# Optimization experiments

Hardware: AMD Instinct MI355X
Metric: run time of the kernel (lower is better)

## Reference

```python
import jax, jax.numpy as jnp
import numpy as np

N_NODES = 50000


def setup_inputs() -> dict:
    key = jax.random.key(0)
    k1, k2, k3, k4, k5 = jax.random.split(key, 5)
    h = jax.random.normal(k1, (50000, 256), dtype=jnp.float32)
    norm = jax.random.uniform(k2, (50000, 1), dtype=jnp.float32)
    weight = jax.random.normal(k3, (256, 96), dtype=jnp.float32) * (1.0 / np.sqrt(96.0))
    src = jax.random.randint(k4, (800000,), 0, N_NODES, dtype=jnp.int64)
    dst = jax.random.randint(k5, (800000,), 0, N_NODES, dtype=jnp.int64)
    return {"h": h, "norm": norm, "weight": weight, "src": src, "dst": dst}


def reference(h, norm, weight, src, dst):
    # dense projection: [N, in] @ [in, out] -> [N, out]
    hw = jnp.matmul(h, weight)
    # pre-aggregation degree norm
    hw = hw * norm
    # copy_src + sum: gather messages from src, scatter-add into dst
    msgs = hw[src]  # [E, out]
    agg = jax.ops.segment_sum(msgs, dst, num_segments=N_NODES)
    # post-aggregation degree norm + activation
    out = jax.nn.relu(agg * norm)
    return out
```

## Files before the change

kernel.cpp:

```cpp
#include <hip/hip_runtime.h>

#define M_NODES 50000
#define KDIM    256
#define NDIM    96
#define NEDGE   800000
#define BM      64
#define TPB     2
#define GEMM_BLKS 391
#define NPB     64
#define NBUCK   782
#define CAPB    1536
#define EPB     2048
#define NBLK_SC 391
#define TOT_BLKS 782

typedef short bf16x8 __attribute__((ext_vector_type(8)));
typedef float f32x4  __attribute__((ext_vector_type(4)));

__device__ inline unsigned short f2bf(float x) {
    unsigned u = __float_as_uint(x);
    u = (u + 0x7fffu + ((u >> 16) & 1u)) >> 16;
    return (unsigned short)u;
}
__device__ inline unsigned pack2bf(float x, float y) {
    return (unsigned)f2bf(x) | ((unsigned)f2bf(y) << 16);
}

__global__ __launch_bounds__(256) void prep_w_kernel(
    const float* __restrict__ w, unsigned short* __restrict__ wt,
    int* __restrict__ gcursor)
{
    const int b = blockIdx.x, t = threadIdx.x;
    if (b < 96) {
        wt[b * 256 + t] = f2bf(w[(size_t)t * NDIM + b]);
    } else {
        for (int i = t; i < NBUCK; i += 256) gcursor[i] = i * CAPB;
    }
}

__global__ __launch_bounds__(256) void fused_gemm_scatter_kernel(
    const float* __restrict__ h, const float* __restrict__ norm,
    const unsigned short* __restrict__ wt, unsigned short* __restrict__ hwb,
    const int* __restrict__ src, const int* __restrict__ dst,
    int* __restrict__ gcursor, unsigned* __restrict__ binned)
{
    __shared__ __align__(16) char smem[81920];

    const int tid = threadIdx.x;
    const unsigned bx = blockIdx.x;

    if ((bx & 1) == 0) {
        const int g = (int)(bx >> 1);
        char* w_lds = smem;
        char* a_lds = smem + 49152 + (tid >> 6) * 8192;
        const int lane = tid & 63;
        const int wv   = tid >> 6;

#pragma unroll
        for (int it = 0; it < 12; ++it) {
            int idx = tid + it * 256;
            int n   = idx >> 5;
            int kb  = (idx & 31) * 16;
            uint4 v = *reinterpret_cast<const uint4*>(
                reinterpret_cast<const char*>(wt) + n * 512 + kb);
            *reinterpret_cast<uint4*>(w_lds + n * 512 + (kb ^ ((n & 7) << 4))) = v;
        }
        __syncthreads();

        const int r16 = lane & 15;
        const int kg  = lane >> 4;

        for (int t = 0; t < TPB; ++t) {
            const int row0 = g * (BM * TPB) + t * BM + wv * 16;

#pragma unroll
            for (int it = 0; it < 8; ++it) {
                int flat = it * 64 + lane;
                int r    = flat >> 5;
                int u    = flat & 31;
                int grow = row0 + r;
                if (grow >= M_NODES) grow = M_NODES - 1;
                const float* hp = h + (size_t)grow * KDIM + u * 8;
                float4 p = *reinterpret_cast<const float4*>(hp);
                float4 q = *reinterpret_cast<const float4*>(hp + 4);
                uint4 o;
                o.x = pack2bf(p.x, p.y); o.y = pack2bf(p.z, p.w);
                o.z = pack2bf(q.x, q.y); o.w = pack2bf(q.z, q.w);
                *reinterpret_cast<uint4*>(
                    a_lds + r * 512 + ((u * 16) ^ ((r & 7) << 4))) = o;
            }

            f32x4 acc[6];
#pragma unroll
            for (int f = 0; f < 6; ++f) acc[f] = (f32x4){0.f, 0.f, 0.f, 0.f};

#pragma unroll
            for (int s = 0; s < 8; ++s) {
                const int kb = s * 64 + kg * 16;
                bf16x8 a = *reinterpret_cast<const bf16x8*>(
                    a_lds + r16 * 512 + (kb ^ ((r16 & 7) << 4)));
#pragma unroll
                for (int f = 0; f < 6; ++f) {
                    int n = f * 16 + (lane & 15);
                    bf16x8 b = *reinterpret_cast<const bf16x8*>(
                        w_lds + n * 512 + (kb ^ ((n & 7) << 4)));
                    acc[f] = __builtin_amdgcn_mfma_f32_16x16x32_bf16(a, b, acc[f], 0, 0, 0);
                }
            }

            const int crow = row0 + (lane >> 4) * 4;
            const int ccol = lane & 15;
#pragma unroll
            for (int r = 0; r < 4; ++r) {
                int row = crow + r;
                if (row < M_NODES) {
                    float nv = norm[row];
#pragma unroll
                    for (int f = 0; f < 6; ++f)
                        hwb[(size_t)row * NDIM + f * 16 + ccol] = f2bf(acc[f][r] * nv);
                }
            }
        }
    } else {
        int* s_cnt  = reinterpret_cast<int*>(smem);
        int* s_base = s_cnt + NBUCK;
        const int blk = (int)(bx >> 1);
        const int e0 = blk * EPB;
        const int e1 = (e0 + EPB < NEDGE) ? e0 + EPB : NEDGE;

        for (int i = tid; i < NBUCK; i += 256) s_cnt[i] = 0;
        __syncthreads();
        for (int e = e0 + tid; e < e1; e += 256)
            atomicAdd(&s_cnt[dst[e] >> 6], 1);
        __syncthreads();
        for (int i = tid; i < NBUCK; i += 256) {
            int c = s_cnt[i];
            s_base[i] = c ? atomicAdd(&gcursor[i], c) : 0;
        }
        __syncthreads();
        for (int i = tid; i < NBUCK; i += 256) s_cnt[i] = 0;
        __syncthreads();
        for (int e = e0 + tid; e < e1; e += 256) {
            int d = dst[e];
            int b = d >> 6;
            int pos = s_base[b] + atomicAdd(&s_cnt[b], 1);
            if (pos < (b + 1) * CAPB)
                binned[pos] = ((unsigned)(d & 63) << 16) | (unsigned)src[e];
        }
    }
}

#define ACCV(A, v)                                     \
    A[0] += __uint_as_float((v).x << 16);              \
    A[1] += __uint_as_float((v).x & 0xffff0000u);      \
    A[2] += __uint_as_float((v).y << 16);              \
    A[3] += __uint_as_float((v).y & 0xffff0000u);      \
    A[4] += __uint_as_float((v).z << 16);              \
    A[5] += __uint_as_float((v).z & 0xffff0000u);      \
    A[6] += __uint_as_float((v).w << 16);              \
    A[7] += __uint_as_float((v).w & 0xffff0000u);

__global__ __launch_bounds__(768) void csr_agg_kernel(
    const unsigned* __restrict__ binned, const int* __restrict__ gcursor,
    const unsigned short* __restrict__ hwb, const float* __restrict__ norm,
    float* __restrict__ out)
{
    __shared__ unsigned eL[CAPB];
    __shared__ unsigned short oL[CAPB];
    __shared__ int cnt[NPB];
    __shared__ int pfxE[NPB];

    const int b  = blockIdx.x;
    const int t  = threadIdx.x;
    const int e0 = b * CAPB;
    int cntE = gcursor[b] - e0;
    if (cntE > CAPB) cntE = CAPB;

    for (int i = t; i < cntE; i += 768) eL[i] = binned[e0 + i];
    if (t < NPB) cnt[t] = 0;
    __syncthreads();
    for (int i = t; i < cntE; i += 768)
        atomicAdd(&cnt[(eL[i] >> 16) & 63], 1);
    __syncthreads();
    if (t < NPB) {
        int v = cnt[t];
        int x = v;
#pragma unroll
        for (int st = 1; st < 64; st <<= 1) {
            int o = __shfl_up(x, st, 64);
            if (t >= st) x += o;
        }
        int ex = x - v;
        pfxE[t] = ex;
        cnt[t]  = ex;
    }
    __syncthreads();
    for (int i = t; i < cntE; i += 768) {
        unsigned v = eL[i];
        int d = (v >> 16) & 63;
        int p = atomicAdd(&cnt[d], 1);
        oL[p] = (unsigned short)(v & 0xffffu);
    }
    __syncthreads();

    const int node  = t / 12;
    const int c8    = t - node * 12;
    const int gnode = b * NPB + node;
    if (gnode < M_NODES) {
        const int s0 = pfxE[node];
        const int s1 = cnt[node];
        float acc[8]  = {0.f, 0.f, 0.f, 0.f, 0.f, 0.f, 0.f, 0.f};
        float acc2[8] = {0.f, 0.f, 0.f, 0.f, 0.f, 0.f, 0.f, 0.f};
        int e = s0;
        for (; e + 4 <= s1; e += 4) {
            int a0 = oL[e], a1 = oL[e + 1], a2 = oL[e + 2], a3 = oL[e + 3];
            uint4 v0 = *reinterpret_cast<const uint4*>(hwb + (size_t)a0 * NDIM + c8 * 8);
            uint4 v1 = *reinterpret_cast<const uint4*>(hwb + (size_t)a1 * NDIM + c8 * 8);
            uint4 v2 = *reinterpret_cast<const uint4*>(hwb + (size_t)a2 * NDIM + c8 * 8);
            uint4 v3 = *reinterpret_cast<const uint4*>(hwb + (size_t)a3 * NDIM + c8 * 8);
            ACCV(acc, v0); ACCV(acc2, v1); ACCV(acc, v2); ACCV(acc2, v3);
        }
        for (; e < s1; ++e) {
            int a0 = oL[e];
            uint4 v0 = *reinterpret_cast<const uint4*>(hwb + (size_t)a0 * NDIM + c8 * 8);
            ACCV(acc, v0);
        }
        const float nv = norm[gnode];
        float4 o0, o1;
        o0.x = fmaxf((acc[0] + acc2[0]) * nv, 0.f);
        o0.y = fmaxf((acc[1] + acc2[1]) * nv, 0.f);
        o0.z = fmaxf((acc[2] + acc2[2]) * nv, 0.f);
        o0.w = fmaxf((acc[3] + acc2[3]) * nv, 0.f);
        o1.x = fmaxf((acc[4] + acc2[4]) * nv, 0.f);
        o1.y = fmaxf((acc[5] + acc2[5]) * nv, 0.f);
        o1.z = fmaxf((acc[6] + acc2[6]) * nv, 0.f);
        o1.w = fmaxf((acc[7] + acc2[7]) * nv, 0.f);
        float4* po = reinterpret_cast<float4*>(out + (size_t)gnode * NDIM + c8 * 8);
        po[0] = o0; po[1] = o1;
    }
}

extern "C" void kernel_launch(void* const* d_in, const int* in_sizes, int n_in,
                              void* d_out, int out_size, void* d_ws, size_t ws_size,
                              hipStream_t stream)
{
    const float* h    = (const float*)d_in[0];
    const float* norm = (const float*)d_in[1];
    const float* w    = (const float*)d_in[2];
    const int*   src  = (const int*)d_in[3];
    const int*   dst  = (const int*)d_in[4];
    float* out = (float*)d_out;

    unsigned short* hwb = (unsigned short*)d_ws;
    unsigned short* wt  = hwb + (size_t)M_NODES * NDIM;
    int* gcursor = (int*)(wt + KDIM * NDIM);
    unsigned* binned = (unsigned*)(gcursor + 800);

    prep_w_kernel<<<97, 256, 0, stream>>>(w, wt, gcursor);
    fused_gemm_scatter_kernel<<<TOT_BLKS, 256, 0, stream>>>(
        h, norm, wt, hwb, src, dst, gcursor, binned);
    csr_agg_kernel<<<NBUCK, 768, 0, stream>>>(binned, gcursor, hwb, norm, out);
}
```

Before: 63.34 us.

## Load A fragments directly from global into registers, process two row tiles per wave

The GEMM path stops staging the converted h tile in LDS and has each lane load its MFMA A fragment straight from global memory, converting to bf16 in registers. Each wave now computes two 16-row tiles at once, so every B fragment read from LDS feeds two MFMAs. This drops the per-wave A staging buffer, shrinking LDS from 80KB to 48KB, which may allow more blocks per CU. In exchange, global loads become strided 32-byte chunks per lane instead of coalesced row reads, and register pressure rises with twelve accumulators.

```diff
diff --git a/kernel.cpp b/kernel.cpp
--- a/kernel.cpp
+++ b/kernel.cpp
@@ -4,8 +4,7 @@
 #define KDIM    256
 #define NDIM    96
 #define NEDGE   800000
-#define BM      64
-#define TPB     2
+#define BMB     128
 #define GEMM_BLKS 391
 #define NPB     64
 #define NBUCK   782
@@ -44,7 +43,7 @@
     const int* __restrict__ src, const int* __restrict__ dst,
     int* __restrict__ gcursor, unsigned* __restrict__ binned)
 {
-    __shared__ __align__(16) char smem[81920];
+    __shared__ __align__(16) char smem[49152];
 
     const int tid = threadIdx.x;
     const unsigned bx = blockIdx.x;
@@ -52,9 +51,11 @@
     if ((bx & 1) == 0) {
         const int g = (int)(bx >> 1);
         char* w_lds = smem;
-        char* a_lds = smem + 49152 + (tid >> 6) * 8192;
         const int lane = tid & 63;
         const int wv   = tid >> 6;
+        const int r16  = lane & 15;
+        const int kg   = lane >> 4;
+        const int row0 = g * BMB + wv * 32;
 
 #pragma unroll
         for (int it = 0; it < 12; ++it) {
@@ -67,58 +68,60 @@
         }
         __syncthreads();
 
-        const int r16 = lane & 15;
-        const int kg  = lane >> 4;
-
-        for (int t = 0; t < TPB; ++t) {
-            const int row0 = g * (BM * TPB) + t * BM + wv * 16;
-
-#pragma unroll
-            for (int it = 0; it < 8; ++it) {
-                int flat = it * 64 + lane;
-                int r    = flat >> 5;
-                int u    = flat & 31;
-                int grow = row0 + r;
-                if (grow >= M_NODES) grow = M_NODES - 1;
-                const float* hp = h + (size_t)grow * KDIM + u * 8;
-                float4 p = *reinterpret_cast<const float4*>(hp);
-                float4 q = *reinterpret_cast<const float4*>(hp + 4);
-                uint4 o;
-                o.x = pack2bf(p.x, p.y); o.y = pack2bf(p.z, p.w);
-                o.z = pack2bf(q.x, q.y); o.w = pack2bf(q.z, q.w);
-                *reinterpret_cast<uint4*>(
-                    a_lds + r * 512 + ((u * 16) ^ ((r & 7) << 4))) = o;
+        int ar0 = row0 + r16;
+        int ar1 = row0 + 16 + r16;
+        if (ar0 >= M_NODES) ar0 = M_NODES - 1;
+        if (ar1 >= M_NODES) ar1 = M_NODES - 1;
+        const float* __restrict__ hp0 = h + (size_t)ar0 * KDIM + kg * 8;
+        const float* __restrict__ hp1 = h + (size_t)ar1 * KDIM + kg * 8;
+
+        f32x4 acc0[6], acc1[6];
+#pragma unroll
+        for (int f = 0; f < 6; ++f) {
+            acc0[f] = (f32x4){0.f, 0.f, 0.f, 0.f};
+            acc1[f] = (f32x4){0.f, 0.f, 0.f, 0.f};
+        }
+
+#pragma unroll
+        for (int s = 0; s < 8; ++s) {
+            float4 p0 = *reinterpret_cast<const float4*>(hp0 + s * 32);
+            float4 q0 = *reinterpret_cast<const float4*>(hp0 + s * 32 + 4);
+            float4 p1 = *reinterpret_cast<const float4*>(hp1 + s * 32);
+            float4 q1 = *reinterpret_cast<const float4*>(hp1 + s * 32 + 4);
+            union { bf16x8 v; unsigned u[4]; } a0, a1;
+            a0.u[0] = pack2bf(p0.x, p0.y); a0.u[1] = pack2bf(p0.z, p0.w);
+            a0.u[2] = pack2bf(q0.x, q0.y); a0.u[3] = pack2bf(q0.z, q0.w);
+            a1.u[0] = pack2bf(p1.x, p1.y); a1.u[1] = pack2bf(p1.z, p1.w);
+            a1.u[2] = pack2bf(q1.x, q1.y); a1.u[3] = pack2bf(q1.z, q1.w);
+
+            const int kb = s * 64 + kg * 16;
+#pragma unroll
+            for (int f = 0; f < 6; ++f) {
+                int n = f * 16 + (lane & 15);
+                bf16x8 b = *reinterpret_cast<const bf16x8*>(
+                    w_lds + n * 512 + (kb ^ ((n & 7) << 4)));
+                acc0[f] = __builtin_amdgcn_mfma_f32_16x16x32_bf16(a0.v, b, acc0[f], 0, 0, 0);
+                acc1[f] = __builtin_amdgcn_mfma_f32_16x16x32_bf16(a1.v, b, acc1[f], 0, 0, 0);
             }
-
-            f32x4 acc[6];
-#pragma unroll
-            for (int f = 0; f < 6; ++f) acc[f] = (f32x4){0.f, 0.f, 0.f, 0.f};
-
-#pragma unroll
-            for (int s = 0; s < 8; ++s) {
-                const int kb = s * 64 + kg * 16;
-                bf16x8 a = *reinterpret_cast<const bf16x8*>(
-                    a_lds + r16 * 512 + (kb ^ ((r16 & 7) << 4)));
-#pragma unroll
-                for (int f = 0; f < 6; ++f) {
-                    int n = f * 16 + (lane & 15);
-                    bf16x8 b = *reinterpret_cast<const bf16x8*>(
-                        w_lds + n * 512 + (kb ^ ((n & 7) << 4)));
-                    acc[f] = __builtin_amdgcn_mfma_f32_16x16x32_bf16(a, b, acc[f], 0, 0, 0);
-                }
+        }
+
+        const int crow = (lane >> 4) * 4;
+        const int ccol = lane & 15;
+#pragma unroll
+        for (int r = 0; r < 4; ++r) {
+            int rowA = row0 + crow + r;
+            if (rowA < M_NODES) {
+                float nv = norm[rowA];
+#pragma unroll
+                for (int f = 0; f < 6; ++f)
+                    hwb[(size_t)rowA * NDIM + f * 16 + ccol] = f2bf(acc0[f][r] * nv);
             }
-
-            const int crow = row0 + (lane >> 4) * 4;
-            const int ccol = lane & 15;
-#pragma unroll
-            for (int r = 0; r < 4; ++r) {
-                int row = crow + r;
-                if (row < M_NODES) {
-                    float nv = norm[row];
-#pragma unroll
-                    for (int f = 0; f < 6; ++f)
-                        hwb[(size_t)row * NDIM + f * 16 + ccol] = f2bf(acc[f][r] * nv);
-                }
+            int rowB = row0 + 16 + crow + r;
+            if (rowB < M_NODES) {
+                float nv = norm[rowB];
+#pragma unroll
+                for (int f = 0; f < 6; ++f)
+                    hwb[(size_t)rowB * NDIM + f * 16 + ccol] = f2bf(acc1[f][r] * nv);
             }
         }
     } else {
```

New measurement: 68.01 us. 1.07x slower.
